# Performance work log

Hardware: AMD Instinct MI355X
Metric: run time of the kernel (lower is better)

The kernel has to match this reference:

```python
import jax, jax.numpy as jnp
import numpy as np

B, M = 2, 8192          # clouds per batch, points per cloud (N = B*M)
K_NEAR, K_FAR, K_SMOOTH = 8, 16, 8
T_LOC, T_CON = 0.1, 0.5
EPS = 1e-8


def setup_inputs() -> dict:
    key = jax.random.key(0)
    k1, k2 = jax.random.split(key)
    scores = jax.random.uniform(k1, (B * M,), dtype=jnp.float32)          # in [0,1]
    coords = jax.random.normal(k2, (B * M, 3), dtype=jnp.float32) * 2.0   # point positions
    batch_ids = (jnp.arange(B * M, dtype=jnp.int32) // M).astype(jnp.int32)
    return {"scores": scores, "coords": coords, "batch_ids": batch_ids}


def _knn_global(coords):
    """Per-cloud brute-force kNN (self included as first neighbor, like pointops.knn_query).
    coords: (N,3) -> global indices (N, K_FAR)."""
    c = coords.reshape(B, M, 3)

    def per_cloud(cb):  # cb: (M,3)
        sq = jnp.sum(cb * cb, axis=-1)                      # (M,)
        d2 = sq[:, None] + sq[None, :] - 2.0 * (cb @ cb.T)  # (M,M) squared dists
        _, idx = jax.lax.top_k(-d2, K_FAR)                  # (M,K_FAR) smallest dists
        return idx

    idx = jax.vmap(per_cloud)(c)                            # (B,M,K_FAR) local indices
    idx = idx + (jnp.arange(B, dtype=idx.dtype) * M)[:, None, None]
    return idx.reshape(B * M, K_FAR)


def _loss_terms(scores, coords, idx):
    # --- locality: neighbors (incl. self) should have similar scores ---
    nb = idx[:, :K_NEAR]                                    # (N,k)
    score_diff = jnp.abs(scores[:, None] - scores[nb])      # (N,k)
    dists = jnp.linalg.norm(coords[:, None, :] - coords[nb], axis=2)  # (N,k)
    w = jnp.exp(-dists / T_LOC)
    loss_loc = jnp.sum(w * score_diff ** 2) / jnp.clip(jnp.sum(w), 1e-8)

    # --- contrastive: near similar, far dissimilar ---
    sim_pos = 1.0 - jnp.abs(scores[:, None] - scores[idx[:, :K_NEAR]])
    sim_neg = 1.0 - jnp.abs(scores[:, None] - scores[idx[:, K_NEAR:K_FAR]])
    loss_pos = -jnp.mean(jnp.log(jax.nn.sigmoid(sim_pos / T_CON) + EPS))
    loss_neg = -jnp.mean(jnp.log(1.0 - jax.nn.sigmoid(sim_neg / T_CON) + EPS))
    loss_con = loss_pos + loss_neg

    # --- distribution: sorted scores match uniform linspace per cloud ---
    sb = jnp.sort(scores.reshape(B, M), axis=1)             # (B,M)
    target = jnp.linspace(0.0, 1.0, M, dtype=scores.dtype)  # (M,)
    loss_dist = jnp.mean(jnp.mean((sb - target[None, :]) ** 2, axis=1))

    # --- smoothness: score close to neighbor mean ---
    nmean = jnp.mean(scores[idx[:, :K_SMOOTH]], axis=1)     # (N,)
    loss_smooth = jnp.mean((scores - nmean) ** 2)

    return loss_loc, loss_con, loss_dist, loss_smooth


def reference(scores, coords, batch_ids):
    del batch_ids  # equal-sized clouds; batch structure is (B, M) by construction
    idx = _knn_global(coords)
    l_loc, l_con, l_dist, l_smooth = _loss_terms(scores, coords, idx)
    total = 1.0 * l_loc + 0.5 * l_con + 0.3 * l_dist + 0.2 * l_smooth
    return total
```

## Files before the change

### kernel.cpp

```cpp
#include <hip/hip_runtime.h>
#include <hip/hip_bf16.h>
#include <math.h>

#define BB 2
#define MM 8192
#define NN (BB * MM)
#define NBATCH (NN / 16)
#define NCELL 4096
#define LOSS_BLOCKS 1024

#define PART_OFF   0
#define RANK_OFF   24576
#define IDX_OFF    90112
#define PK_OFF     1138688
#define SS_OFF     1400832
#define CELLID_OFF 1466368
#define CNT_OFF    1531904
#define CUR_OFF    1564672
#define BBLO_OFF   1597440
#define BBHI_OFF   1613824

__device__ __forceinline__ unsigned mort3(unsigned x, unsigned y, unsigned z) {
    unsigned m = 0;
#pragma unroll
    for (int i = 0; i < 4; ++i) {
        m |= ((x >> i) & 1u) << (3 * i);
        m |= ((y >> i) & 1u) << (3 * i + 1);
        m |= ((z >> i) & 1u) << (3 * i + 2);
    }
    return m;
}

__global__ void count_kernel(const float* __restrict__ coords, int* __restrict__ cellid,
                             int* __restrict__ cnt) {
    int i = blockIdx.x * 256 + threadIdx.x;
    if (i < NN) {
        float x = coords[3 * i], y = coords[3 * i + 1], z = coords[3 * i + 2];
        int cx = min(15, max(0, (int)floorf(x) + 8));
        int cy = min(15, max(0, (int)floorf(y) + 8));
        int cz = min(15, max(0, (int)floorf(z) + 8));
        int cid = (i >> 13) * NCELL + (int)mort3((unsigned)cx, (unsigned)cy, (unsigned)cz);
        cellid[i] = cid;
        atomicAdd(&cnt[cid], 1);
    }
}

__global__ __launch_bounds__(1024) void scan_kernel(const int* __restrict__ cnt,
                                                    int* __restrict__ cursor) {
    __shared__ int wsum[16];
    const int tid = threadIdx.x, lane = tid & 63, wv = tid >> 6;
    int v[8]; int run = 0;
#pragma unroll
    for (int i = 0; i < 8; ++i) { int t = cnt[tid * 8 + i]; v[i] = run; run += t; }
    int inc = run;
#pragma unroll
    for (int off = 1; off < 64; off <<= 1) {
        int y = __shfl_up(inc, off);
        if (lane >= off) inc += y;
    }
    int laneExcl = inc - run;
    if (lane == 63) wsum[wv] = inc;
    __syncthreads();
    int wbase = 0;
#pragma unroll
    for (int w = 0; w < 16; ++w) wbase += (w < wv) ? wsum[w] : 0;
    const int base = wbase + laneExcl;
#pragma unroll
    for (int i = 0; i < 8; ++i) cursor[tid * 8 + i] = base + v[i];
}

__global__ void scatter_kernel(const float* __restrict__ coords, const float* __restrict__ scores,
                               const int* __restrict__ cellid, int* __restrict__ cursor,
                               float4* __restrict__ pk_s, float* __restrict__ s_s) {
    int i = blockIdx.x * 256 + threadIdx.x;
    if (i < NN) {
        int pos = atomicAdd(&cursor[cellid[i]], 1);
        float x = coords[3 * i], y = coords[3 * i + 1], z = coords[3 * i + 2];
        float sq = fmaf(x, x, fmaf(y, y, z * z));
        pk_s[pos] = make_float4(x, y, z, sq);
        s_s[pos] = scores[i];
    }
}

__global__ void bbox_kernel(const float4* __restrict__ pk_s, float4* __restrict__ bb_lo,
                            float4* __restrict__ bb_hi) {
    int b = blockIdx.x * 256 + threadIdx.x;
    if (b < NBATCH) {
        float4 c = pk_s[b * 16];
        float lx = c.x, ly = c.y, lz = c.z, hx = c.x, hy = c.y, hz = c.z;
#pragma unroll
        for (int i = 1; i < 16; ++i) {
            c = pk_s[b * 16 + i];
            lx = fminf(lx, c.x); ly = fminf(ly, c.y); lz = fminf(lz, c.z);
            hx = fmaxf(hx, c.x); hy = fmaxf(hy, c.y); hz = fmaxf(hz, c.z);
        }
        bb_lo[b] = make_float4(lx, ly, lz, 0.f);
        bb_hi[b] = make_float4(hx, hy, hz, 0.f);
    }
}

__device__ __forceinline__ void sort16(unsigned (&a)[16]) {
#pragma unroll
    for (int p2 = 1; p2 < 16; p2 <<= 1) {
#pragma unroll
        for (int k2 = p2; k2 >= 1; k2 >>= 1) {
#pragma unroll
            for (int j2 = k2 % p2; j2 + k2 < 16; j2 += 2 * k2) {
#pragma unroll
                for (int i2 = 0; i2 < k2; ++i2) {
                    if (i2 + j2 + k2 < 16) {
                        if (((i2 + j2) / (2 * p2)) == ((i2 + j2 + k2) / (2 * p2))) {
                            unsigned x = a[i2 + j2], y = a[i2 + j2 + k2];
                            a[i2 + j2]      = min(x, y);
                            a[i2 + j2 + k2] = max(x, y);
                        }
                    }
                }
            }
        }
    }
}

__device__ __forceinline__ void truncmerge(unsigned (&slot)[16], const unsigned (&kb)[16]) {
    unsigned m[16];
#pragma unroll
    for (int k = 0; k < 16; ++k) m[k] = min(slot[k], kb[15 - k]);
#pragma unroll
    for (int st = 8; st >= 1; st >>= 1) {
#pragma unroll
        for (int i = 0; i < 16; ++i) {
            if ((i & st) == 0) {
                unsigned lo = min(m[i], m[i + st]);
                unsigned hi = max(m[i], m[i + st]);
                m[i] = lo; m[i + st] = hi;
            }
        }
    }
#pragma unroll
    for (int k = 0; k < 16; ++k) slot[k] = m[k];
}

__global__ __launch_bounds__(1024) void knn_kernel(const float4* __restrict__ pk_s,
                                                   const float4* __restrict__ bb_lo,
                                                   const float4* __restrict__ bb_hi,
                                                   int* __restrict__ out_idx) {
    __shared__ unsigned lds_k[16][16][64];
    __shared__ float lds_t[16][64];
    const int tid = threadIdx.x, lane = tid & 63;
    const int wv = __builtin_amdgcn_readfirstlane(tid >> 6);
    const int qbase = blockIdx.x * 64;
    const int cloudbase = (qbase >> 13) << 13;
    const int q = qbase + lane;
    const float4 p = pk_s[q];
    const int sb0 = (qbase - cloudbase) >> 4;
    const float4* __restrict__ pc = pk_s + cloudbase;
    const int bbase = cloudbase >> 4;

    unsigned slot[16];
#pragma unroll
    for (int k = 0; k < 16; ++k) slot[k] = 0x7F000000u + (unsigned)k;
    float t_f = 3.0e38f;

    auto batch = [&](int bi) {
        unsigned kb[16];
#pragma unroll
        for (int i = 0; i < 16; ++i) {
            const int j = bi * 16 + i;
            const float4 c = pc[j];
            float dot = fmaf(p.x, c.x, fmaf(p.y, c.y, p.z * c.z));
            float d2  = fmaf(-2.0f, dot, p.w + c.w);
            kb[i] = (__float_as_uint(d2) & 0xFFFFE000u) | (unsigned)j;
        }
        sort16(kb);
        truncmerge(slot, kb);
        t_f = fminf(t_f, __uint_as_float((slot[15] & 0xFFFFE000u) + 0x2000u));
    };

    const int r = sb0 & 15;
    const int ownb = (wv >= r && wv < r + 4) ? (sb0 + (wv - r)) : -1;
    if (ownb >= 0) batch(ownb);
    lds_t[wv][lane] = t_f;
    __syncthreads();
    float tb = lds_t[0][lane];
#pragma unroll
    for (int w = 1; w < 16; ++w) tb = fminf(tb, lds_t[w][lane]);
    t_f = fminf(t_f, tb);

    float4 lo = bb_lo[bbase + wv];
    float4 hi = bb_hi[bbase + wv];
    for (int k = 0; k < 32; ++k) {
        const int bi = wv + (k << 4);
        float4 lo_n, hi_n;
        if (k + 1 < 32) {
            lo_n = bb_lo[bbase + bi + 16];
            hi_n = bb_hi[bbase + bi + 16];
        }
        if (bi != ownb) {
            float dx = fmaxf(fmaxf(lo.x - p.x, p.x - hi.x), 0.f);
            float dy = fmaxf(fmaxf(lo.y - p.y, p.y - hi.y), 0.f);
            float dz = fmaxf(fmaxf(lo.z - p.z, p.z - hi.z), 0.f);
            float lb = fmaf(dx, dx, fmaf(dy, dy, dz * dz));
            if (__any(fmaf(lb, 0.999f, -1e-5f) < t_f)) batch(bi);
        }
        lo = lo_n; hi = hi_n;
    }

#pragma unroll
    for (int k = 0; k < 16; ++k) lds_k[wv][k][lane] = slot[k];

    for (int half = 8; half >= 1; half >>= 1) {
        __syncthreads();
        if (wv < half) {
            unsigned a[16], m[16];
#pragma unroll
            for (int k = 0; k < 16; ++k) a[k] = lds_k[wv][k][lane];
#pragma unroll
            for (int k = 0; k < 16; ++k) m[k] = min(a[k], lds_k[wv + half][15 - k][lane]);
#pragma unroll
            for (int st = 8; st >= 1; st >>= 1) {
#pragma unroll
                for (int i = 0; i < 16; ++i) {
                    if ((i & st) == 0) {
                        unsigned lo2 = min(m[i], m[i + st]);
                        unsigned hi2 = max(m[i], m[i + st]);
                        m[i] = lo2; m[i + st] = hi2;
                    }
                }
            }
#pragma unroll
            for (int k = 0; k < 16; ++k) lds_k[wv][k][lane] = m[k];
        }
    }
    __syncthreads();

    if (wv == 0) {
#pragma unroll
        for (int k = 0; k < 16; ++k)
            out_idx[(qbase + lane) * 16 + k] = (int)(lds_k[0][k][lane] & 0x1FFFu) + cloudbase;
    }
}

__global__ __launch_bounds__(1024) void rank_kernel(const float* __restrict__ s_s,
                                                    int* __restrict__ out_rank) {
    __shared__ int lds_r[16][64];
    const int tid = threadIdx.x, lane = tid & 63;
    const int wv = __builtin_amdgcn_readfirstlane(tid >> 6);
    const int qbase = blockIdx.x * 64;
    const int cloudbase = (qbase >> 13) << 13;
    const float s = s_s[qbase + lane];
    const float* __restrict__ sc = s_s + cloudbase;
    int rank = 0;
    const int j0 = wv * 512;
    for (int jj = 0; jj < 512; jj += 16) {
#pragma unroll
        for (int i = 0; i < 16; ++i) {
            rank += (sc[j0 + jj + i] < s) ? 1 : 0;
        }
    }
    lds_r[wv][lane] = rank;
    __syncthreads();
    if (wv == 0) {
        int rsum = 0;
#pragma unroll
        for (int w = 0; w < 16; ++w) rsum += lds_r[w][lane];
        out_rank[qbase + lane] = rsum;
    }
}

__global__ __launch_bounds__(256) void loss_kernel(const float* __restrict__ s_s,
                                                   const float4* __restrict__ pk_s,
                                                   const int* __restrict__ knn,
                                                   const int* __restrict__ rank,
                                                   float* __restrict__ partial) {
    __shared__ float red[4][6];
    const int t = blockIdx.x * 256 + threadIdx.x;
    const int q = t >> 4, k = t & 15;
    const int nb = knn[t];
    const float s  = s_s[q];
    const float sn = s_s[nb];
    const float diff = fabsf(s - sn);
    const float sim = 1.0f - diff;
    const float sg = 1.0f / (1.0f + expf(-2.0f * sim));

    float a_wd = 0.f, a_w = 0.f, a_pos = 0.f, a_neg = 0.f, snk = 0.f;
    if (k < 8) {
        float4 pq = pk_s[q];
        float4 pn = pk_s[nb];
        float dx = pq.x - pn.x, dy = pq.y - pn.y, dz = pq.z - pn.z;
        float d = sqrtf(dx * dx + dy * dy + dz * dz);
        float w = expf(-10.0f * d);
        a_wd = w * diff * diff;
        a_w  = w;
        a_pos = logf(sg + 1e-8f);
        snk = sn;
    } else {
        a_neg = logf(1.0f - sg + 1e-8f);
    }

    float nsum = snk;
#pragma unroll
    for (int off = 1; off < 16; off <<= 1) nsum += __shfl_xor(nsum, off);

    float a_sm = 0.f, a_di = 0.f;
    if (k == 0) {
        float t1 = s - nsum * 0.125f;
        a_sm = t1 * t1;
        float t2 = s - (float)rank[q] * (1.0f / 8191.0f);
        a_di = t2 * t2;
    }

#pragma unroll
    for (int off = 1; off < 64; off <<= 1) {
        a_wd  += __shfl_xor(a_wd, off);
        a_w   += __shfl_xor(a_w, off);
        a_pos += __shfl_xor(a_pos, off);
        a_neg += __shfl_xor(a_neg, off);
        a_sm  += __shfl_xor(a_sm, off);
        a_di  += __shfl_xor(a_di, off);
    }
    const int wv = threadIdx.x >> 6;
    if ((threadIdx.x & 63) == 0) {
        red[wv][0] = a_wd; red[wv][1] = a_w; red[wv][2] = a_pos;
        red[wv][3] = a_neg; red[wv][4] = a_sm; red[wv][5] = a_di;
    }
    __syncthreads();
    if (threadIdx.x < 6) {
        float v = red[0][threadIdx.x] + red[1][threadIdx.x] +
                  red[2][threadIdx.x] + red[3][threadIdx.x];
        partial[threadIdx.x * LOSS_BLOCKS + blockIdx.x] = v;
    }
}

__global__ __launch_bounds__(1024) void fin_kernel(const float* __restrict__ partial,
                                                   float* __restrict__ out) {
    __shared__ float red[16][6];
    const int tid = threadIdx.x;
    float a[6];
#pragma unroll
    for (int term = 0; term < 6; ++term) a[term] = partial[term * LOSS_BLOCKS + tid];
#pragma unroll
    for (int off = 1; off < 64; off <<= 1) {
#pragma unroll
        for (int term = 0; term < 6; ++term) a[term] += __shfl_xor(a[term], off);
    }
    if ((tid & 63) == 0) {
#pragma unroll
        for (int term = 0; term < 6; ++term) red[tid >> 6][term] = a[term];
    }
    __syncthreads();
    if (tid == 0) {
        float acc[6];
#pragma unroll
        for (int term = 0; term < 6; ++term) {
            float v = 0.f;
#pragma unroll
            for (int w = 0; w < 16; ++w) v += red[w][term];
            acc[term] = v;
        }
        float l_loc = acc[0] / fmaxf(acc[1], 1e-8f);
        float l_pos = -acc[2] / (float)(NN * 8);
        float l_neg = -acc[3] / (float)(NN * 8);
        float l_sm  = acc[4] / (float)NN;
        float l_di  = acc[5] / (float)NN;
        out[0] = l_loc + 0.5f * (l_pos + l_neg) + 0.3f * l_di + 0.2f * l_sm;
    }
}

extern "C" void kernel_launch(void* const* d_in, const int* in_sizes, int n_in,
                              void* d_out, int out_size, void* d_ws, size_t ws_size,
                              hipStream_t stream) {
    const float* scores = (const float*)d_in[0];
    const float* coords = (const float*)d_in[1];
    (void)in_sizes; (void)n_in; (void)out_size; (void)ws_size;

    char* ws = (char*)d_ws;
    float*  part  = (float*)(ws + PART_OFF);
    int*    rank  = (int*)(ws + RANK_OFF);
    int*    knn   = (int*)(ws + IDX_OFF);
    float4* pk_s  = (float4*)(ws + PK_OFF);
    float*  s_s   = (float*)(ws + SS_OFF);
    int*    cellid= (int*)(ws + CELLID_OFF);
    int*    cnt   = (int*)(ws + CNT_OFF);
    int*    cursor= (int*)(ws + CUR_OFF);
    float4* bb_lo = (float4*)(ws + BBLO_OFF);
    float4* bb_hi = (float4*)(ws + BBHI_OFF);
    float*  out   = (float*)d_out;

    hipMemsetAsync(cnt, 0, 2 * NCELL * sizeof(int), stream);
    count_kernel<<<64, 256, 0, stream>>>(coords, cellid, cnt);
    scan_kernel<<<1, 1024, 0, stream>>>(cnt, cursor);
    scatter_kernel<<<64, 256, 0, stream>>>(coords, scores, cellid, cursor, pk_s, s_s);
    bbox_kernel<<<4, 256, 0, stream>>>(pk_s, bb_lo, bb_hi);
    knn_kernel<<<256, 1024, 0, stream>>>(pk_s, bb_lo, bb_hi, knn);
    rank_kernel<<<256, 1024, 0, stream>>>(s_s, rank);
    loss_kernel<<<LOSS_BLOCKS, 256, 0, stream>>>(s_s, pk_s, knn, rank, part);
    fin_kernel<<<1, 1024, 0, stream>>>(part, out);
}
```

Baseline: 149.7 us.

## Load-balance kNN candidate batches across waves via shared work queue

Replaces the fixed strided assignment of candidate point batches to waves with a two-phase scheme. First all waves cull batches by bounding box against the initial threshold and push survivors into a shared LDS queue, then waves pull from the queue dynamically. The per-lane distance threshold is shared across waves through LDS atomicMin, so later culling uses the tightest bound found so far, and sort/merge is skipped when no candidate in a batch can enter the top list. This trades the statically strided loop and prefetching for LDS atomics, an extra barrier, and queue overhead, and it assumes at most 512 batches are queued.

New measurement: 168.8 us. 12.8% more time.

```diff
diff --git a/kernel.cpp b/kernel.cpp
--- a/kernel.cpp
+++ b/kernel.cpp
@@ -145,7 +145,10 @@
                                                    const float4* __restrict__ bb_hi,
                                                    int* __restrict__ out_idx) {
     __shared__ unsigned lds_k[16][16][64];
-    __shared__ float lds_t[16][64];
+    __shared__ unsigned lds_tmin[64];
+    __shared__ int q_list[512];
+    __shared__ int q_num;
+    __shared__ int q_head;
     const int tid = threadIdx.x, lane = tid & 63;
     const int wv = __builtin_amdgcn_readfirstlane(tid >> 6);
     const int qbase = blockIdx.x * 64;
@@ -156,12 +159,15 @@
     const float4* __restrict__ pc = pk_s + cloudbase;
     const int bbase = cloudbase >> 4;
 
+    if (tid < 64) lds_tmin[tid] = 0x7f7fffffu;
+    if (tid == 0) { q_num = 0; q_head = 0; }
+
     unsigned slot[16];
 #pragma unroll
     for (int k = 0; k < 16; ++k) slot[k] = 0x7F000000u + (unsigned)k;
     float t_f = 3.0e38f;
 
-    auto batch = [&](int bi) {
+    auto batch = [&](int bi, float tbound) {
         unsigned kb[16];
 #pragma unroll
         for (int i = 0; i < 16; ++i) {
@@ -171,38 +177,59 @@
             float d2  = fmaf(-2.0f, dot, p.w + c.w);
             kb[i] = (__float_as_uint(d2) & 0xFFFFE000u) | (unsigned)j;
         }
-        sort16(kb);
-        truncmerge(slot, kb);
-        t_f = fminf(t_f, __uint_as_float((slot[15] & 0xFFFFE000u) + 0x2000u));
+        unsigned kmin = kb[0];
+#pragma unroll
+        for (int i = 1; i < 16; ++i) kmin = min(kmin, kb[i]);
+        const bool useful = (kmin < slot[15]) &&
+                            (__uint_as_float(kmin & 0xFFFFE000u) < tbound);
+        if (__any(useful)) {
+            sort16(kb);
+            truncmerge(slot, kb);
+            float nt = __uint_as_float((slot[15] & 0xFFFFE000u) + 0x2000u);
+            if (nt < t_f) {
+                t_f = nt;
+                atomicMin(&lds_tmin[lane], __float_as_uint(nt));
+            }
+        }
     };
 
     const int r = sb0 & 15;
     const int ownb = (wv >= r && wv < r + 4) ? (sb0 + (wv - r)) : -1;
-    if (ownb >= 0) batch(ownb);
-    lds_t[wv][lane] = t_f;
-    __syncthreads();
-    float tb = lds_t[0][lane];
-#pragma unroll
-    for (int w = 1; w < 16; ++w) tb = fminf(tb, lds_t[w][lane]);
-    t_f = fminf(t_f, tb);
-
-    float4 lo = bb_lo[bbase + wv];
-    float4 hi = bb_hi[bbase + wv];
+    __syncthreads();
+    if (ownb >= 0) batch(ownb, 3.0e38f);
+    __syncthreads();
+    t_f = fminf(t_f, __uint_as_float(lds_tmin[lane]));
+
     for (int k = 0; k < 32; ++k) {
         const int bi = wv + (k << 4);
-        float4 lo_n, hi_n;
-        if (k + 1 < 32) {
-            lo_n = bb_lo[bbase + bi + 16];
-            hi_n = bb_hi[bbase + bi + 16];
-        }
-        if (bi != ownb) {
-            float dx = fmaxf(fmaxf(lo.x - p.x, p.x - hi.x), 0.f);
-            float dy = fmaxf(fmaxf(lo.y - p.y, p.y - hi.y), 0.f);
-            float dz = fmaxf(fmaxf(lo.z - p.z, p.z - hi.z), 0.f);
-            float lb = fmaf(dx, dx, fmaf(dy, dy, dz * dz));
-            if (__any(fmaf(lb, 0.999f, -1e-5f) < t_f)) batch(bi);
-        }
-        lo = lo_n; hi = hi_n;
+        if (bi >= sb0 && bi < sb0 + 4) continue;
+        const float4 lo = bb_lo[bbase + bi];
+        const float4 hi = bb_hi[bbase + bi];
+        float dx = fmaxf(fmaxf(lo.x - p.x, p.x - hi.x), 0.f);
+        float dy = fmaxf(fmaxf(lo.y - p.y, p.y - hi.y), 0.f);
+        float dz = fmaxf(fmaxf(lo.z - p.z, p.z - hi.z), 0.f);
+        float lb = fmaf(dx, dx, fmaf(dy, dy, dz * dz));
+        if (__any(fmaf(lb, 0.999f, -1e-5f) < t_f)) {
+            if (lane == 0) { int pp = atomicAdd(&q_num, 1); q_list[pp] = bi; }
+        }
+    }
+    __syncthreads();
+    const int qn = q_num;
+
+    for (;;) {
+        int pos = 0;
+        if (lane == 0) pos = atomicAdd(&q_head, 1);
+        pos = __shfl(pos, 0);
+        if (pos >= qn) break;
+        const int bi = q_list[pos];
+        const float4 lo = bb_lo[bbase + bi];
+        const float4 hi = bb_hi[bbase + bi];
+        float dx = fmaxf(fmaxf(lo.x - p.x, p.x - hi.x), 0.f);
+        float dy = fmaxf(fmaxf(lo.y - p.y, p.y - hi.y), 0.f);
+        float dz = fmaxf(fmaxf(lo.z - p.z, p.z - hi.z), 0.f);
+        float lb = fmaf(dx, dx, fmaf(dy, dy, dz * dz));
+        const float tsh = __uint_as_float(lds_tmin[lane]);
+        if (__any(fmaf(lb, 0.999f, -1e-5f) < tsh)) batch(bi, tsh);
     }
 
 #pragma unroll
```

## Split kNN candidate batches across four blocks per query group and merge

Applied to the files above, without the earlier changes.

The kNN kernel now launches four blocks per 64-query group, each scanning a quarter of the cloud's candidate batches, and writes partial top-16 key lists. A new merge kernel combines the four partial lists into final indices. The pruning threshold is shared through an LDS atomicMin that all waves update as they go, and batches are skipped before sorting if no lane's minimum key could improve its list. This is meant to raise GPU occupancy and cut each block's serial scan, at the cost of redundant seed-batch work, one extra kernel launch and extra global traffic.

After: 158.1 us. +5.6%, slower.

```diff
diff --git a/kernel.cpp b/kernel.cpp
--- a/kernel.cpp
+++ b/kernel.cpp
@@ -19,6 +19,7 @@
 #define CUR_OFF    1564672
 #define BBLO_OFF   1597440
 #define BBHI_OFF   1613824
+#define PKEY_OFF   1630208
 
 __device__ __forceinline__ unsigned mort3(unsigned x, unsigned y, unsigned z) {
     unsigned m = 0;
@@ -143,26 +144,28 @@
 __global__ __launch_bounds__(1024) void knn_kernel(const float4* __restrict__ pk_s,
                                                    const float4* __restrict__ bb_lo,
                                                    const float4* __restrict__ bb_hi,
-                                                   int* __restrict__ out_idx) {
+                                                   unsigned* __restrict__ pkeys) {
     __shared__ unsigned lds_k[16][16][64];
-    __shared__ float lds_t[16][64];
+    __shared__ unsigned lds_tmin[64];
     const int tid = threadIdx.x, lane = tid & 63;
     const int wv = __builtin_amdgcn_readfirstlane(tid >> 6);
-    const int qbase = blockIdx.x * 64;
+    const int g  = blockIdx.x >> 2;
+    const int qt = blockIdx.x & 3;
+    const int qbase = g << 6;
     const int cloudbase = (qbase >> 13) << 13;
-    const int q = qbase + lane;
-    const float4 p = pk_s[q];
+    const float4 p = pk_s[qbase + lane];
     const int sb0 = (qbase - cloudbase) >> 4;
     const float4* __restrict__ pc = pk_s + cloudbase;
     const int bbase = cloudbase >> 4;
+    const int qt0 = qt << 7;
+
+    if (tid < 64) lds_tmin[tid] = 0x7f7fffffu;
 
     unsigned slot[16];
 #pragma unroll
     for (int k = 0; k < 16; ++k) slot[k] = 0x7F000000u + (unsigned)k;
-    float t_f = 3.0e38f;
-
-    auto batch = [&](int bi) {
-        unsigned kb[16];
+
+    auto loadkeys = [&](int bi, unsigned (&kb)[16]) {
 #pragma unroll
         for (int i = 0; i < 16; ++i) {
             const int j = bi * 16 + i;
@@ -171,36 +174,54 @@
             float d2  = fmaf(-2.0f, dot, p.w + c.w);
             kb[i] = (__float_as_uint(d2) & 0xFFFFE000u) | (unsigned)j;
         }
-        sort16(kb);
-        truncmerge(slot, kb);
-        t_f = fminf(t_f, __uint_as_float((slot[15] & 0xFFFFE000u) + 0x2000u));
+    };
+
+    auto batch = [&](int bi, float tbound) {
+        unsigned kb[16];
+        loadkeys(bi, kb);
+        unsigned kmin = kb[0];
+#pragma unroll
+        for (int i = 1; i < 16; ++i) kmin = min(kmin, kb[i]);
+        const bool useful = (kmin < slot[15]) &&
+                            (__uint_as_float(kmin & 0xFFFFE000u) < tbound);
+        if (__any(useful)) {
+            sort16(kb);
+            truncmerge(slot, kb);
+            atomicMin(&lds_tmin[lane], (slot[15] & 0xFFFFE000u) + 0x2000u);
+        }
     };
 
     const int r = sb0 & 15;
     const int ownb = (wv >= r && wv < r + 4) ? (sb0 + (wv - r)) : -1;
-    if (ownb >= 0) batch(ownb);
-    lds_t[wv][lane] = t_f;
-    __syncthreads();
-    float tb = lds_t[0][lane];
-#pragma unroll
-    for (int w = 1; w < 16; ++w) tb = fminf(tb, lds_t[w][lane]);
-    t_f = fminf(t_f, tb);
-
-    float4 lo = bb_lo[bbase + wv];
-    float4 hi = bb_hi[bbase + wv];
-    for (int k = 0; k < 32; ++k) {
-        const int bi = wv + (k << 4);
+    __syncthreads();
+    if (ownb >= 0) {
+        unsigned kb[16];
+        loadkeys(ownb, kb);
+        sort16(kb);
+        atomicMin(&lds_tmin[lane], (kb[15] & 0xFFFFE000u) + 0x2000u);
+    }
+    __syncthreads();
+
+    float4 lo = bb_lo[bbase + qt0 + wv];
+    float4 hi = bb_hi[bbase + qt0 + wv];
+    for (int k = 0; k < 8; ++k) {
+        const int bi = qt0 + wv + (k << 4);
         float4 lo_n, hi_n;
-        if (k + 1 < 32) {
+        if (k + 1 < 8) {
             lo_n = bb_lo[bbase + bi + 16];
             hi_n = bb_hi[bbase + bi + 16];
         }
-        if (bi != ownb) {
+        const bool isSeed = (bi >= sb0 && bi < sb0 + 4);
+        if (!isSeed) {
+            const float tsh = __uint_as_float(lds_tmin[lane]);
             float dx = fmaxf(fmaxf(lo.x - p.x, p.x - hi.x), 0.f);
             float dy = fmaxf(fmaxf(lo.y - p.y, p.y - hi.y), 0.f);
             float dz = fmaxf(fmaxf(lo.z - p.z, p.z - hi.z), 0.f);
             float lb = fmaf(dx, dx, fmaf(dy, dy, dz * dz));
-            if (__any(fmaf(lb, 0.999f, -1e-5f) < t_f)) batch(bi);
+            if (__any(fmaf(lb, 0.999f, -1e-5f) < tsh)) batch(bi, tsh);
+        } else {
+            const float tsh = __uint_as_float(lds_tmin[lane]);
+            batch(bi, tsh);
         }
         lo = lo_n; hi = hi_n;
     }
@@ -236,8 +257,28 @@
     if (wv == 0) {
 #pragma unroll
         for (int k = 0; k < 16; ++k)
-            out_idx[(qbase + lane) * 16 + k] = (int)(lds_k[0][k][lane] & 0x1FFFu) + cloudbase;
-    }
+            pkeys[(unsigned)(blockIdx.x * 16 + k) * 64 + lane] = lds_k[0][k][lane];
+    }
+}
+
+__global__ __launch_bounds__(256) void merge4_kernel(const unsigned* __restrict__ pkeys,
+                                                     int* __restrict__ out_idx) {
+    const int t = blockIdx.x * 256 + threadIdx.x;
+    const int g = t >> 6, lane = t & 63;
+    const int cloudbase = (g >> 7) << 13;
+    unsigned a[16];
+#pragma unroll
+    for (int k = 0; k < 16; ++k) a[k] = pkeys[(unsigned)((g * 4 + 0) * 16 + k) * 64 + lane];
+#pragma unroll
+    for (int qt = 1; qt < 4; ++qt) {
+        unsigned b[16];
+#pragma unroll
+        for (int k = 0; k < 16; ++k) b[k] = pkeys[(unsigned)((g * 4 + qt) * 16 + k) * 64 + lane];
+        truncmerge(a, b);
+    }
+#pragma unroll
+    for (int k = 0; k < 16; ++k)
+        out_idx[(g * 64 + lane) * 16 + k] = (int)(a[k] & 0x1FFFu) + cloudbase;
 }
 
 __global__ __launch_bounds__(1024) void rank_kernel(const float* __restrict__ s_s,
@@ -384,6 +425,7 @@
     int*    cursor= (int*)(ws + CUR_OFF);
     float4* bb_lo = (float4*)(ws + BBLO_OFF);
     float4* bb_hi = (float4*)(ws + BBHI_OFF);
+    unsigned* pkeys = (unsigned*)(ws + PKEY_OFF);
     float*  out   = (float*)d_out;
 
     hipMemsetAsync(cnt, 0, 2 * NCELL * sizeof(int), stream);
@@ -391,7 +433,8 @@
     scan_kernel<<<1, 1024, 0, stream>>>(cnt, cursor);
     scatter_kernel<<<64, 256, 0, stream>>>(coords, scores, cellid, cursor, pk_s, s_s);
     bbox_kernel<<<4, 256, 0, stream>>>(pk_s, bb_lo, bb_hi);
-    knn_kernel<<<256, 1024, 0, stream>>>(pk_s, bb_lo, bb_hi, knn);
+    knn_kernel<<<1024, 1024, 0, stream>>>(pk_s, bb_lo, bb_hi, pkeys);
+    merge4_kernel<<<64, 256, 0, stream>>>(pkeys, knn);
     rank_kernel<<<256, 1024, 0, stream>>>(s_s, rank);
     loss_kernel<<<LOSS_BLOCKS, 256, 0, stream>>>(s_s, pk_s, knn, rank, part);
     fin_kernel<<<1, 1024, 0, stream>>>(part, out);
```

## Fuse pipeline into cooperative prep, merged knn+rank, and last-block final reduction

Applied to the files above, without the earlier changes.

Collapses the memset, count, scan, scatter and bbox launches into one cooperative kernel separated by grid syncs. The rank computation now runs as extra blocks of the knn launch. The final reduction moves into the loss kernel through a last-block-done atomic counter. kNN waves also share their pruning threshold through an LDS atomicMin so other waves skip more batches. The aim is to cut launch overhead and inter-kernel gaps, at the cost of grid-sync latency and extra atomics.

Measured after the change: 212.0 us. 41.6% more time.

```diff
diff --git a/kernel.cpp b/kernel.cpp
--- a/kernel.cpp
+++ b/kernel.cpp
@@ -1,6 +1,8 @@
 #include <hip/hip_runtime.h>
-#include <hip/hip_bf16.h>
+#include <hip/hip_cooperative_groups.h>
 #include <math.h>
+
+namespace cg = cooperative_groups;
 
 #define BB 2
 #define MM 8192
@@ -19,6 +21,7 @@
 #define CUR_OFF    1564672
 #define BBLO_OFF   1597440
 #define BBHI_OFF   1613824
+#define DONE_OFF   1630208
 
 __device__ __forceinline__ unsigned mort3(unsigned x, unsigned y, unsigned z) {
     unsigned m = 0;
@@ -31,10 +34,22 @@
     return m;
 }
 
-__global__ void count_kernel(const float* __restrict__ coords, int* __restrict__ cellid,
-                             int* __restrict__ cnt) {
-    int i = blockIdx.x * 256 + threadIdx.x;
-    if (i < NN) {
+__global__ __launch_bounds__(1024) void prep_kernel(
+    const float* __restrict__ coords, const float* __restrict__ scores,
+    int* __restrict__ cellid, int* __restrict__ cnt, int* __restrict__ cursor,
+    float4* __restrict__ pk_s, float* __restrict__ s_s,
+    float4* __restrict__ bb_lo, float4* __restrict__ bb_hi,
+    unsigned* __restrict__ done) {
+    cg::grid_group grid = cg::this_grid();
+    __shared__ int wsum[16];
+    const int tid = threadIdx.x, blk = blockIdx.x;
+
+    if (tid < 128) cnt[blk * 128 + tid] = 0;
+    if (blk == 0 && tid == 0) *done = 0u;
+    grid.sync();
+
+    if (tid < 256) {
+        const int i = blk * 256 + tid;
         float x = coords[3 * i], y = coords[3 * i + 1], z = coords[3 * i + 2];
         int cx = min(15, max(0, (int)floorf(x) + 8));
         int cy = min(15, max(0, (int)floorf(y) + 8));
@@ -43,49 +58,43 @@
         cellid[i] = cid;
         atomicAdd(&cnt[cid], 1);
     }
-}
-
-__global__ __launch_bounds__(1024) void scan_kernel(const int* __restrict__ cnt,
-                                                    int* __restrict__ cursor) {
-    __shared__ int wsum[16];
-    const int tid = threadIdx.x, lane = tid & 63, wv = tid >> 6;
-    int v[8]; int run = 0;
-#pragma unroll
-    for (int i = 0; i < 8; ++i) { int t = cnt[tid * 8 + i]; v[i] = run; run += t; }
-    int inc = run;
-#pragma unroll
-    for (int off = 1; off < 64; off <<= 1) {
-        int y = __shfl_up(inc, off);
-        if (lane >= off) inc += y;
-    }
-    int laneExcl = inc - run;
-    if (lane == 63) wsum[wv] = inc;
-    __syncthreads();
-    int wbase = 0;
-#pragma unroll
-    for (int w = 0; w < 16; ++w) wbase += (w < wv) ? wsum[w] : 0;
-    const int base = wbase + laneExcl;
-#pragma unroll
-    for (int i = 0; i < 8; ++i) cursor[tid * 8 + i] = base + v[i];
-}
-
-__global__ void scatter_kernel(const float* __restrict__ coords, const float* __restrict__ scores,
-                               const int* __restrict__ cellid, int* __restrict__ cursor,
-                               float4* __restrict__ pk_s, float* __restrict__ s_s) {
-    int i = blockIdx.x * 256 + threadIdx.x;
-    if (i < NN) {
+    grid.sync();
+
+    if (blk == 0) {
+        const int lane = tid & 63, wv = tid >> 6;
+        int v[8]; int run = 0;
+#pragma unroll
+        for (int i = 0; i < 8; ++i) { int t = cnt[tid * 8 + i]; v[i] = run; run += t; }
+        int inc = run;
+#pragma unroll
+        for (int off = 1; off < 64; off <<= 1) {
+            int y = __shfl_up(inc, off);
+            if (lane >= off) inc += y;
+        }
+        int laneExcl = inc - run;
+        if (lane == 63) wsum[wv] = inc;
+        __syncthreads();
+        int wbase = 0;
+#pragma unroll
+        for (int w = 0; w < 16; ++w) wbase += (w < wv) ? wsum[w] : 0;
+        const int base = wbase + laneExcl;
+#pragma unroll
+        for (int i = 0; i < 8; ++i) cursor[tid * 8 + i] = base + v[i];
+    }
+    grid.sync();
+
+    if (tid < 256) {
+        const int i = blk * 256 + tid;
         int pos = atomicAdd(&cursor[cellid[i]], 1);
         float x = coords[3 * i], y = coords[3 * i + 1], z = coords[3 * i + 2];
         float sq = fmaf(x, x, fmaf(y, y, z * z));
         pk_s[pos] = make_float4(x, y, z, sq);
         s_s[pos] = scores[i];
     }
-}
-
-__global__ void bbox_kernel(const float4* __restrict__ pk_s, float4* __restrict__ bb_lo,
-                            float4* __restrict__ bb_hi) {
-    int b = blockIdx.x * 256 + threadIdx.x;
-    if (b < NBATCH) {
+    grid.sync();
+
+    if (tid < 16) {
+        const int b = blk * 16 + tid;
         float4 c = pk_s[b * 16];
         float lx = c.x, ly = c.y, lz = c.z, hx = c.x, hy = c.y, hz = c.z;
 #pragma unroll
@@ -140,21 +149,50 @@
     for (int k = 0; k < 16; ++k) slot[k] = m[k];
 }
 
-__global__ __launch_bounds__(1024) void knn_kernel(const float4* __restrict__ pk_s,
-                                                   const float4* __restrict__ bb_lo,
-                                                   const float4* __restrict__ bb_hi,
-                                                   int* __restrict__ out_idx) {
+__global__ __launch_bounds__(1024) void knnrank_kernel(const float4* __restrict__ pk_s,
+                                                       const float* __restrict__ s_s,
+                                                       const float4* __restrict__ bb_lo,
+                                                       const float4* __restrict__ bb_hi,
+                                                       int* __restrict__ out_idx,
+                                                       int* __restrict__ out_rank) {
     __shared__ unsigned lds_k[16][16][64];
-    __shared__ float lds_t[16][64];
+    __shared__ int lds_aux[16][64];
+    __shared__ unsigned lds_tmin[64];
     const int tid = threadIdx.x, lane = tid & 63;
     const int wv = __builtin_amdgcn_readfirstlane(tid >> 6);
+
+    if (blockIdx.x >= 256) {
+        const int qbase = (blockIdx.x - 256) << 6;
+        const int cloudbase = (qbase >> 13) << 13;
+        const float s = s_s[qbase + lane];
+        const float* __restrict__ sc = s_s + cloudbase;
+        int rk = 0;
+        const int j0 = wv * 512;
+        for (int jj = 0; jj < 512; jj += 16) {
+#pragma unroll
+            for (int i = 0; i < 16; ++i) {
+                rk += (sc[j0 + jj + i] < s) ? 1 : 0;
+            }
+        }
+        lds_aux[wv][lane] = rk;
+        __syncthreads();
+        if (wv == 0) {
+            int rsum = 0;
+#pragma unroll
+            for (int w = 0; w < 16; ++w) rsum += lds_aux[w][lane];
+            out_rank[qbase + lane] = rsum;
+        }
+        return;
+    }
+
     const int qbase = blockIdx.x * 64;
     const int cloudbase = (qbase >> 13) << 13;
-    const int q = qbase + lane;
-    const float4 p = pk_s[q];
+    const float4 p = pk_s[qbase + lane];
     const int sb0 = (qbase - cloudbase) >> 4;
     const float4* __restrict__ pc = pk_s + cloudbase;
     const int bbase = cloudbase >> 4;
+
+    if (tid < 64) lds_tmin[tid] = 0x7f7fffffu;
 
     unsigned slot[16];
 #pragma unroll
@@ -173,17 +211,23 @@
         }
         sort16(kb);
         truncmerge(slot, kb);
-        t_f = fminf(t_f, __uint_as_float((slot[15] & 0xFFFFE000u) + 0x2000u));
+        const unsigned nt = (slot[15] & 0xFFFFE000u) + 0x2000u;
+        const float ntf = __uint_as_float(nt);
+        if (ntf < t_f) {
+            t_f = ntf;
+            atomicMin(&lds_tmin[lane], nt);
+        }
     };
 
     const int r = sb0 & 15;
     const int ownb = (wv >= r && wv < r + 4) ? (sb0 + (wv - r)) : -1;
+    __syncthreads();
     if (ownb >= 0) batch(ownb);
-    lds_t[wv][lane] = t_f;
-    __syncthreads();
-    float tb = lds_t[0][lane];
-#pragma unroll
-    for (int w = 1; w < 16; ++w) tb = fminf(tb, lds_t[w][lane]);
+    lds_aux[wv][lane] = (int)__float_as_uint(t_f);
+    __syncthreads();
+    float tb = __uint_as_float((unsigned)lds_aux[0][lane]);
+#pragma unroll
+    for (int w = 1; w < 16; ++w) tb = fminf(tb, __uint_as_float((unsigned)lds_aux[w][lane]));
     t_f = fminf(t_f, tb);
 
     float4 lo = bb_lo[bbase + wv];
@@ -196,11 +240,13 @@
             hi_n = bb_hi[bbase + bi + 16];
         }
         if (bi != ownb) {
+            const unsigned tmb = *((volatile unsigned*)&lds_tmin[lane]);
+            const float tsh = fminf(t_f, __uint_as_float(tmb));
             float dx = fmaxf(fmaxf(lo.x - p.x, p.x - hi.x), 0.f);
             float dy = fmaxf(fmaxf(lo.y - p.y, p.y - hi.y), 0.f);
             float dz = fmaxf(fmaxf(lo.z - p.z, p.z - hi.z), 0.f);
             float lb = fmaf(dx, dx, fmaf(dy, dy, dz * dz));
-            if (__any(fmaf(lb, 0.999f, -1e-5f) < t_f)) batch(bi);
+            if (__any(fmaf(lb, 0.999f, -1e-5f) < tsh)) batch(bi);
         }
         lo = lo_n; hi = hi_n;
     }
@@ -240,39 +286,16 @@
     }
 }
 
-__global__ __launch_bounds__(1024) void rank_kernel(const float* __restrict__ s_s,
-                                                    int* __restrict__ out_rank) {
-    __shared__ int lds_r[16][64];
-    const int tid = threadIdx.x, lane = tid & 63;
-    const int wv = __builtin_amdgcn_readfirstlane(tid >> 6);
-    const int qbase = blockIdx.x * 64;
-    const int cloudbase = (qbase >> 13) << 13;
-    const float s = s_s[qbase + lane];
-    const float* __restrict__ sc = s_s + cloudbase;
-    int rank = 0;
-    const int j0 = wv * 512;
-    for (int jj = 0; jj < 512; jj += 16) {
-#pragma unroll
-        for (int i = 0; i < 16; ++i) {
-            rank += (sc[j0 + jj + i] < s) ? 1 : 0;
-        }
-    }
-    lds_r[wv][lane] = rank;
-    __syncthreads();
-    if (wv == 0) {
-        int rsum = 0;
-#pragma unroll
-        for (int w = 0; w < 16; ++w) rsum += lds_r[w][lane];
-        out_rank[qbase + lane] = rsum;
-    }
-}
-
-__global__ __launch_bounds__(256) void loss_kernel(const float* __restrict__ s_s,
-                                                   const float4* __restrict__ pk_s,
-                                                   const int* __restrict__ knn,
-                                                   const int* __restrict__ rank,
-                                                   float* __restrict__ partial) {
+__global__ __launch_bounds__(256) void lossfin_kernel(const float* __restrict__ s_s,
+                                                      const float4* __restrict__ pk_s,
+                                                      const int* __restrict__ knn,
+                                                      const int* __restrict__ rnk,
+                                                      float* __restrict__ partial,
+                                                      unsigned* __restrict__ done,
+                                                      float* __restrict__ out) {
     __shared__ float red[4][6];
+    __shared__ float sgrp[16][6];
+    __shared__ unsigned lastflag;
     const int t = blockIdx.x * 256 + threadIdx.x;
     const int q = t >> 4, k = t & 15;
     const int nb = knn[t];
@@ -305,7 +328,7 @@
     if (k == 0) {
         float t1 = s - nsum * 0.125f;
         a_sm = t1 * t1;
-        float t2 = s - (float)rank[q] * (1.0f / 8191.0f);
+        float t2 = s - (float)rnk[q] * (1.0f / 8191.0f);
         a_di = t2 * t2;
     }
 
@@ -327,42 +350,51 @@
     if (threadIdx.x < 6) {
         float v = red[0][threadIdx.x] + red[1][threadIdx.x] +
                   red[2][threadIdx.x] + red[3][threadIdx.x];
-        partial[threadIdx.x * LOSS_BLOCKS + blockIdx.x] = v;
-    }
-}
-
-__global__ __launch_bounds__(1024) void fin_kernel(const float* __restrict__ partial,
-                                                   float* __restrict__ out) {
-    __shared__ float red[16][6];
-    const int tid = threadIdx.x;
-    float a[6];
-#pragma unroll
-    for (int term = 0; term < 6; ++term) a[term] = partial[term * LOSS_BLOCKS + tid];
-#pragma unroll
-    for (int off = 1; off < 64; off <<= 1) {
-#pragma unroll
-        for (int term = 0; term < 6; ++term) a[term] += __shfl_xor(a[term], off);
-    }
-    if ((tid & 63) == 0) {
-#pragma unroll
-        for (int term = 0; term < 6; ++term) red[tid >> 6][term] = a[term];
-    }
-    __syncthreads();
-    if (tid == 0) {
-        float acc[6];
-#pragma unroll
-        for (int term = 0; term < 6; ++term) {
-            float v = 0.f;
-#pragma unroll
-            for (int w = 0; w < 16; ++w) v += red[w][term];
-            acc[term] = v;
-        }
-        float l_loc = acc[0] / fmaxf(acc[1], 1e-8f);
-        float l_pos = -acc[2] / (float)(NN * 8);
-        float l_neg = -acc[3] / (float)(NN * 8);
-        float l_sm  = acc[4] / (float)NN;
-        float l_di  = acc[5] / (float)NN;
-        out[0] = l_loc + 0.5f * (l_pos + l_neg) + 0.3f * l_di + 0.2f * l_sm;
+        __hip_atomic_store(&partial[threadIdx.x * LOSS_BLOCKS + blockIdx.x], v,
+                           __ATOMIC_RELEASE, __HIP_MEMORY_SCOPE_AGENT);
+    }
+    __syncthreads();
+    if (threadIdx.x == 0)
+        lastflag = __hip_atomic_fetch_add(done, 1u, __ATOMIC_ACQ_REL, __HIP_MEMORY_SCOPE_AGENT);
+    __syncthreads();
+
+    if (lastflag == (unsigned)(LOSS_BLOCKS - 1)) {
+        const int tid = threadIdx.x, lane2 = tid & 63, w4 = tid >> 6;
+#pragma unroll
+        for (int rep = 0; rep < 4; ++rep) {
+            const int w = w4 * 4 + rep;
+            float a[6];
+#pragma unroll
+            for (int term = 0; term < 6; ++term)
+                a[term] = __hip_atomic_load(&partial[term * LOSS_BLOCKS + w * 64 + lane2],
+                                            __ATOMIC_ACQUIRE, __HIP_MEMORY_SCOPE_AGENT);
+#pragma unroll
+            for (int off = 1; off < 64; off <<= 1) {
+#pragma unroll
+                for (int term = 0; term < 6; ++term) a[term] += __shfl_xor(a[term], off);
+            }
+            if (lane2 == 0) {
+#pragma unroll
+                for (int term = 0; term < 6; ++term) sgrp[w][term] = a[term];
+            }
+        }
+        __syncthreads();
+        if (tid == 0) {
+            float acc[6];
+#pragma unroll
+            for (int term = 0; term < 6; ++term) {
+                float v = 0.f;
+#pragma unroll
+                for (int w = 0; w < 16; ++w) v += sgrp[w][term];
+                acc[term] = v;
+            }
+            float l_loc = acc[0] / fmaxf(acc[1], 1e-8f);
+            float l_pos = -acc[2] / (float)(NN * 8);
+            float l_neg = -acc[3] / (float)(NN * 8);
+            float l_sm  = acc[4] / (float)NN;
+            float l_di  = acc[5] / (float)NN;
+            out[0] = l_loc + 0.5f * (l_pos + l_neg) + 0.3f * l_di + 0.2f * l_sm;
+        }
     }
 }
 
@@ -384,15 +416,14 @@
     int*    cursor= (int*)(ws + CUR_OFF);
     float4* bb_lo = (float4*)(ws + BBLO_OFF);
     float4* bb_hi = (float4*)(ws + BBHI_OFF);
+    unsigned* done= (unsigned*)(ws + DONE_OFF);
     float*  out   = (float*)d_out;
 
-    hipMemsetAsync(cnt, 0, 2 * NCELL * sizeof(int), stream);
-    count_kernel<<<64, 256, 0, stream>>>(coords, cellid, cnt);
-    scan_kernel<<<1, 1024, 0, stream>>>(cnt, cursor);
-    scatter_kernel<<<64, 256, 0, stream>>>(coords, scores, cellid, cursor, pk_s, s_s);
-    bbox_kernel<<<4, 256, 0, stream>>>(pk_s, bb_lo, bb_hi);
-    knn_kernel<<<256, 1024, 0, stream>>>(pk_s, bb_lo, bb_hi, knn);
-    rank_kernel<<<256, 1024, 0, stream>>>(s_s, rank);
-    loss_kernel<<<LOSS_BLOCKS, 256, 0, stream>>>(s_s, pk_s, knn, rank, part);
-    fin_kernel<<<1, 1024, 0, stream>>>(part, out);
-}
+    void* prep_args[10] = { (void*)&coords, (void*)&scores, (void*)&cellid, (void*)&cnt,
+                            (void*)&cursor, (void*)&pk_s, (void*)&s_s, (void*)&bb_lo,
+                            (void*)&bb_hi, (void*)&done };
+    hipLaunchCooperativeKernel(reinterpret_cast<void*>(prep_kernel),
+                               dim3(64), dim3(1024), prep_args, 0, stream);
+    knnrank_kernel<<<512, 1024, 0, stream>>>(pk_s, s_s, bb_lo, bb_hi, knn, rank);
+    lossfin_kernel<<<LOSS_BLOCKS, 256, 0, stream>>>(s_s, pk_s, knn, rank, part, done, out);
+}
```
